# Optimization experiments

Measured on AMD Instinct MI355X. Metric: run time of the kernel, lower is better.

The kernel has to match this reference:

```python
import jax, jax.numpy as jnp
import numpy as np

B, T, H, I, O = 64, 1024, 512, 64, 8
NOISE_STD = 0.05
ALPHA = 0.2


def setup_inputs() -> dict:
    key = jax.random.key(0)
    ks = jax.random.split(key, 5)
    return {
        "input": jax.random.normal(ks[0], (B, T, I), dtype=jnp.float32),
        "noise": jax.random.normal(ks[1], (B, T, H), dtype=jnp.float32),
        "wi": jax.random.normal(ks[2], (I, H), dtype=jnp.float32) / np.float32(np.sqrt(H)),
        "si": jnp.ones((I,), jnp.float32),
        # scale so the all-positive effective recurrence |wrec| stays stable over T steps
        "wrec": jax.random.normal(ks[3], (H, H), dtype=jnp.float32) * np.float32(0.5 / H),
        "b": jnp.zeros((H,), jnp.float32),
        "wo": jax.random.normal(ks[4], (H, O), dtype=jnp.float32) / np.float32(H),
        "so": jnp.ones((O,), jnp.float32),
        "wi_mask": jnp.ones((I, H), jnp.float32),
        "wrec_mask": jnp.ones((H, H), jnp.float32),
        "wo_mask": jnp.ones((H, O), jnp.float32),
        "h0": jnp.zeros((H,), jnp.float32),
    }


def reference(input, noise, wi, si, wrec, b, wo, so, wi_mask, wrec_mask, wo_mask, h0):
    batch = input.shape[0]
    # effective weights (constant across timesteps; torch recomputes identical values each step)
    wrec_eff = jnp.abs(wrec) * wrec_mask            # [H, H]
    wi_eff = (wi * si[:, None]) * wi_mask           # [I, H]
    wo_eff = (wo * so[None, :]) * wo_mask           # [H, O]

    h_init = jnp.broadcast_to(h0, (batch, h0.shape[0]))  # [B, H]

    def step(h, xs):
        x_t, n_t = xs                                # [B, I], [B, H]
        r = jax.nn.relu(h)                           # rate from previous state
        h_new = h + NOISE_STD * n_t + ALPHA * (-h + r @ wrec_eff + b + x_t @ wi_eff)
        out_t = jax.nn.relu(h_new) @ wo_eff          # [B, O]
        return h_new, (out_t, h_new)

    xs = (jnp.swapaxes(input, 0, 1), jnp.swapaxes(noise, 0, 1))  # time-major
    _, (outs, hs) = jax.lax.scan(step, h_init, xs)
    output = jnp.swapaxes(outs, 0, 1)                            # [B, T, O]
    trajectories = jnp.concatenate(
        [h_init[:, None, :], jnp.swapaxes(hs, 0, 1)], axis=1     # [B, T+1, H]
    )
    return output, trajectories
```

## Files before the change

kernel.cpp:

```cpp
#include <hip/hip_runtime.h>
#include <hip/hip_bf16.h>
#include <cstddef>
#include <cstdint>

#define BB 64
#define TT 1024
#define HH 512
#define II 64
#define OO 8
#define NOISE_STD 0.05f
#define ALPHA 0.2f

#define G_SLICES 16
#define BT 4
#define NC (BB/BT)
#define K4EXT 160
#define R2STRIDE 328

typedef _Float16 half2_t __attribute__((ext_vector_type(2)));
typedef unsigned int uint32;
typedef uint32 uint4_t __attribute__((ext_vector_type(4)));

#if __has_builtin(__builtin_amdgcn_fdot2)
__device__ __forceinline__ float fdot2f(half2_t a, half2_t b, float c) {
    return __builtin_amdgcn_fdot2(a, b, c, false);
}
#else
__device__ __forceinline__ float fdot2f(half2_t a, half2_t b, float c) {
    return c + (float)a[0] * (float)b[0] + (float)a[1] * (float)b[1];
}
#endif

__device__ __forceinline__ half2_t pkrtz(float a, float b) {
    return __builtin_bit_cast(half2_t, __builtin_amdgcn_cvt_pkrtz(a, b));
}

__device__ __forceinline__ uint4_t load4_sc1(const uint32* p) {
    uint4_t v;
    asm volatile("global_load_dwordx4 %0, %1, off sc1\n\t"
                 "s_waitcnt vmcnt(0)"
                 : "=v"(v) : "v"(p) : "memory");
    return v;
}
__device__ __forceinline__ uint4_t load4_sc0(const uint32* p) {
    uint4_t v;
    asm volatile("global_load_dwordx4 %0, %1, off sc0\n\t"
                 "s_waitcnt vmcnt(0)"
                 : "=v"(v) : "v"(p) : "memory");
    return v;
}
__device__ __forceinline__ void store1_plain(uint32* p, uint32 v) {
    asm volatile("global_store_dword %0, %1, off" :: "v"(p), "v"(v) : "memory");
}

__global__ __launch_bounds__(512, 2)
void rnn_clique(const float* __restrict__ input, const float* __restrict__ noise,
                const float* __restrict__ wi, const float* __restrict__ si,
                const float* __restrict__ wrec, const float* __restrict__ bvec,
                const float* __restrict__ wo, const float* __restrict__ so,
                const float* __restrict__ wi_mask, const float* __restrict__ wrec_mask,
                const float* __restrict__ wo_mask, const float* __restrict__ h0,
                uint32* __restrict__ ex, float* __restrict__ out,
                float* __restrict__ traj)
{
    const int tid  = threadIdx.x;
    const int cq   = blockIdx.x & 15;
    const int sl   = blockIdx.x >> 4;
    const int wv   = tid >> 6;
    const int lane = tid & 63;

    __shared__ half2_t w2[K4EXT * 64];
    __shared__ half2_t r2[2][BT][R2STRIDE];
    __shared__ float   part[BT][8][32];
    __shared__ half2_t wo2[256];
    __shared__ int     mode_sh;

    uint32* aux = ex + (size_t)NC * 2 * BT * HH;

    if (tid == 0) {
        uint32 xcc;
        asm volatile("s_getreg_b32 %0, hwreg(HW_REG_XCC_ID)" : "=s"(xcc));
        xcc &= 0xFFu;
        __hip_atomic_store(aux + cq * 16 + sl, (1u << 16) | xcc,
                           __ATOMIC_RELAXED, __HIP_MEMORY_SCOPE_AGENT);
    }

    {
        const int c = tid & 31, kg = tid >> 5;
        const int gc = sl * 32 + c;
        for (int m = 0; m < 10; ++m) {
            int k4 = m * 16 + kg;
            float v[4];
            #pragma unroll
            for (int q = 0; q < 4; ++q) {
                int kap = k4 * 4 + q;
                float x;
                if (kap < HH) {
                    x = fabsf(wrec[(size_t)kap * HH + gc]) * wrec_mask[(size_t)kap * HH + gc];
                } else if (kap < HH + II) {
                    int i = kap - HH;
                    x = wi[(size_t)i * HH + gc] * si[i] * wi_mask[(size_t)i * HH + gc];
                } else if (kap == HH + II) {
                    x = bvec[gc];
                } else {
                    x = 0.f;
                }
                v[q] = x;
            }
            w2[k4 * 64 + c * 2]     = pkrtz(v[0], v[1]);
            w2[k4 * 64 + c * 2 + 1] = pkrtz(v[2], v[3]);
        }
    }
    if (sl < OO && tid < 256) {
        int k2 = tid, o = sl;
        float v0 = wo[(size_t)(2 * k2) * OO + o] * so[o] * wo_mask[(size_t)(2 * k2) * OO + o];
        float v1 = wo[(size_t)(2 * k2 + 1) * OO + o] * so[o] * wo_mask[(size_t)(2 * k2 + 1) * OO + o];
        wo2[k2] = pkrtz(v0, v1);
    }
    if (tid < 128) {
        int k4 = tid;
        float v0 = fmaxf(h0[4 * k4 + 0], 0.f), v1 = fmaxf(h0[4 * k4 + 1], 0.f);
        float v2 = fmaxf(h0[4 * k4 + 2], 0.f), v3 = fmaxf(h0[4 * k4 + 3], 0.f);
        half2_t p0 = pkrtz(v0, v1), p1 = pkrtz(v2, v3);
        for (int b = 0; b < BT; ++b) { r2[0][b][2 * k4] = p0; r2[0][b][2 * k4 + 1] = p1; }
    }
    if (tid < 8) {
        int par = tid & 1, b = tid >> 1;
        r2[par][b][288] = half2_t{(_Float16)1.f, (_Float16)0.f};
        for (int s = 289; s < R2STRIDE; ++s) r2[par][b][s] = half2_t{(_Float16)0.f, (_Float16)0.f};
    }
    if (wv >= 4 && lane < 32) {
        int b = wv - 4, i2 = lane;
        const float* xp = input + ((size_t)(cq * BT + b) * TT + 0) * II + 2 * i2;
        r2[0][b][256 + i2] = pkrtz(xp[0], xp[1]);
    }

    float h_st = 0.f, n_reg = 0.f, n_reg2 = 0.f;
    float* trajp = nullptr;
    const float* noisep = nullptr;
    uint32* exw = nullptr;
    if (wv < BT && lane < 32) {
        int b = wv, c = lane, gc = sl * 32 + c, bg = cq * BT + b;
        h_st   = h0[gc];
        noisep = noise + (size_t)bg * TT * HH;
        trajp  = traj + (size_t)bg * (TT + 1) * HH;
        n_reg  = noisep[gc];
        n_reg2 = noisep[(size_t)HH + gc];
        trajp[gc] = h_st;
        exw = ex + (size_t)(cq * 2 * BT + b) * HH + gc;
    }
    __syncthreads();

    const int c_    = lane & 31;
    const int shalf = lane >> 5;
    const int seg   = wv * 2 + shalf;

    half2_t wr[5][4];
    #pragma unroll
    for (int ch = 0; ch < 5; ++ch) {
        int k4b = seg * 10 + ch * 2;
        wr[ch][0] = w2[k4b * 64 + c_ * 2];
        wr[ch][1] = w2[k4b * 64 + c_ * 2 + 1];
        wr[ch][2] = w2[(k4b + 1) * 64 + c_ * 2];
        wr[ch][3] = w2[(k4b + 1) * 64 + c_ * 2 + 1];
    }

    if (wv == 0) {
        uint32 v = (1u << 16);
        for (;;) {
            if (lane < 16)
                v = __hip_atomic_load(aux + cq * 16 + lane,
                                      __ATOMIC_RELAXED, __HIP_MEMORY_SCOPE_AGENT);
            if (__ballot((v >> 16) == 1u) == ~0ull) break;
            __builtin_amdgcn_s_sleep(1);
        }
        uint32 myx = v & 0xFFFFu;
        uint32 x0  = __shfl(myx, 0);
        bool eq = (lane < 16) ? (myx == x0) : true;
        if (lane == 0) mode_sh = (__ballot(eq) == ~0ull) ? 1 : 0;
    }
    __syncthreads();
    const bool local_mode = (mode_sh != 0);

    const int gb  = tid >> 7;
    const int k4g = tid & 127;
    uint32* exg0 = ex + (size_t)(cq * 2 * BT + gb) * HH + (size_t)(4 * k4g);
    const size_t expar = (size_t)BT * HH;

    for (int t = 0; t < TT; ++t) {
        const int p = t & 1;

        float acc0 = 0.f, acc1 = 0.f, acc2 = 0.f, acc3 = 0.f;
        #pragma unroll
        for (int ch = 0; ch < 5; ++ch) {
            int k2b = seg * 20 + ch * 4;
            {
                half2_t ra = r2[p][0][k2b], rb = r2[p][0][k2b + 1], rc = r2[p][0][k2b + 2], rd = r2[p][0][k2b + 3];
                acc0 = fdot2f(ra, wr[ch][0], acc0); acc0 = fdot2f(rb, wr[ch][1], acc0);
                acc0 = fdot2f(rc, wr[ch][2], acc0); acc0 = fdot2f(rd, wr[ch][3], acc0);
            }
            {
                half2_t ra = r2[p][1][k2b], rb = r2[p][1][k2b + 1], rc = r2[p][1][k2b + 2], rd = r2[p][1][k2b + 3];
                acc1 = fdot2f(ra, wr[ch][0], acc1); acc1 = fdot2f(rb, wr[ch][1], acc1);
                acc1 = fdot2f(rc, wr[ch][2], acc1); acc1 = fdot2f(rd, wr[ch][3], acc1);
            }
            {
                half2_t ra = r2[p][2][k2b], rb = r2[p][2][k2b + 1], rc = r2[p][2][k2b + 2], rd = r2[p][2][k2b + 3];
                acc2 = fdot2f(ra, wr[ch][0], acc2); acc2 = fdot2f(rb, wr[ch][1], acc2);
                acc2 = fdot2f(rc, wr[ch][2], acc2); acc2 = fdot2f(rd, wr[ch][3], acc2);
            }
            {
                half2_t ra = r2[p][3][k2b], rb = r2[p][3][k2b + 1], rc = r2[p][3][k2b + 2], rd = r2[p][3][k2b + 3];
                acc3 = fdot2f(ra, wr[ch][0], acc3); acc3 = fdot2f(rb, wr[ch][1], acc3);
                acc3 = fdot2f(rc, wr[ch][2], acc3); acc3 = fdot2f(rd, wr[ch][3], acc3);
            }
        }
        acc0 += __shfl_xor(acc0, 32);
        acc1 += __shfl_xor(acc1, 32);
        acc2 += __shfl_xor(acc2, 32);
        acc3 += __shfl_xor(acc3, 32);
        if (shalf == 0) {
            part[0][wv][c_] = acc0;
            part[1][wv][c_] = acc1;
            part[2][wv][c_] = acc2;
            part[3][wv][c_] = acc3;
        }
        __syncthreads();

        const uint32 tag = (uint32)(t + 2);
        const size_t poff = (size_t)p * expar;

        if (wv < BT && lane < 32) {
            int b = wv, c = lane, gc = sl * 32 + c;
            float mv = 0.f;
            #pragma unroll
            for (int m = 0; m < 8; ++m) mv += part[b][m][c];
            float hn = (1.f - ALPHA) * h_st + ALPHA * mv + NOISE_STD * n_reg;
            h_st = hn;
            uint32 r16 = __builtin_bit_cast(uint32,
                           __builtin_amdgcn_cvt_pkrtz(fmaxf(hn, 0.f), 0.f)) & 0xFFFFu;
            uint32 word = (tag << 16) | r16;
            if (local_mode) {
                store1_plain(exw + poff, word);
            } else {
                __hip_atomic_store(exw + poff, word,
                                   __ATOMIC_RELAXED, __HIP_MEMORY_SCOPE_AGENT);
            }
            trajp[(size_t)(t + 1) * HH + gc] = hn;
            n_reg = n_reg2;
            int tn = (t + 2 < TT) ? (t + 2) : (TT - 1);
            n_reg2 = noisep[(size_t)tn * HH + gc];
        } else if (wv >= 4) {
            if (sl < OO && t > 0) {
                int b = wv - 4;
                int k2 = lane * 4;
                float q = 0.f;
                q = fdot2f(r2[p][b][k2],     wo2[k2],     q);
                q = fdot2f(r2[p][b][k2 + 1], wo2[k2 + 1], q);
                q = fdot2f(r2[p][b][k2 + 2], wo2[k2 + 2], q);
                q = fdot2f(r2[p][b][k2 + 3], wo2[k2 + 3], q);
                #pragma unroll
                for (int d = 32; d >= 1; d >>= 1) q += __shfl_xor(q, d);
                if (lane == 0) out[((size_t)(cq * BT + b) * TT + (t - 1)) * OO + sl] = q;
            }
            if (lane < 32) {
                int b = wv - 4, i2 = lane;
                int tn = (t + 1 < TT) ? (t + 1) : (TT - 1);
                const float* xp = input + ((size_t)(cq * BT + b) * TT + tn) * II + 2 * i2;
                r2[p ^ 1][b][256 + i2] = pkrtz(xp[0], xp[1]);
            }
        }

        {
            const uint32* g0 = exg0 + poff;
            uint4_t w;
            int spins = 0;
            if (local_mode) {
                for (;;) {
                    w = load4_sc0(g0);
                    if ((w[0] >> 16) == tag && (w[1] >> 16) == tag &&
                        (w[2] >> 16) == tag && (w[3] >> 16) == tag) break;
                    if (++spins > 8) __builtin_amdgcn_s_sleep(1);
                }
            } else {
                for (;;) {
                    w = load4_sc1(g0);
                    if ((w[0] >> 16) == tag && (w[1] >> 16) == tag &&
                        (w[2] >> 16) == tag && (w[3] >> 16) == tag) break;
                    __builtin_amdgcn_s_sleep(1);
                }
            }
            uint32 q0 = (w[0] & 0xFFFFu) | (w[1] << 16);
            uint32 q1 = (w[2] & 0xFFFFu) | (w[3] << 16);
            r2[p ^ 1][gb][2 * k4g]     = __builtin_bit_cast(half2_t, q0);
            r2[p ^ 1][gb][2 * k4g + 1] = __builtin_bit_cast(half2_t, q1);
        }
        __syncthreads();
    }

    if (wv >= 4 && sl < OO) {
        int b = wv - 4;
        int k2 = lane * 4;
        float q = 0.f;
        q = fdot2f(r2[0][b][k2],     wo2[k2],     q);
        q = fdot2f(r2[0][b][k2 + 1], wo2[k2 + 1], q);
        q = fdot2f(r2[0][b][k2 + 2], wo2[k2 + 2], q);
        q = fdot2f(r2[0][b][k2 + 3], wo2[k2 + 3], q);
        #pragma unroll
        for (int d = 32; d >= 1; d >>= 1) q += __shfl_xor(q, d);
        if (lane == 0) out[((size_t)(cq * BT + b) * TT + (TT - 1)) * OO + sl] = q;
    }
}

extern "C" void kernel_launch(void* const* d_in, const int* in_sizes, int n_in,
                              void* d_out, int out_size, void* d_ws, size_t ws_size,
                              hipStream_t stream) {
    const float* input     = (const float*)d_in[0];
    const float* noise     = (const float*)d_in[1];
    const float* wi        = (const float*)d_in[2];
    const float* si        = (const float*)d_in[3];
    const float* wrec      = (const float*)d_in[4];
    const float* bvec      = (const float*)d_in[5];
    const float* wo        = (const float*)d_in[6];
    const float* so        = (const float*)d_in[7];
    const float* wi_mask   = (const float*)d_in[8];
    const float* wrec_mask = (const float*)d_in[9];
    const float* wo_mask   = (const float*)d_in[10];
    const float* h0        = (const float*)d_in[11];

    float* out  = (float*)d_out;
    float* traj = out + (size_t)BB * TT * OO;
    uint32* ex  = (uint32*)d_ws;

    (void)hipMemsetAsync(d_ws, 0,
        (size_t)(NC * 2 * BT * HH + NC * G_SLICES) * sizeof(uint32), stream);

    rnn_clique<<<dim3(NC * G_SLICES), dim3(512), 0, stream>>>(
        input, noise, wi, si, wrec, bvec, wo, so,
        wi_mask, wrec_mask, wo_mask, h0, ex, out, traj);
}
```

Measured before the change: 1.602 ms.

## Offload noise, input and trajectory traffic to helper waves and use lighter barriers

```diff
diff --git a/kernel.cpp b/kernel.cpp
--- a/kernel.cpp
+++ b/kernel.cpp
@@ -33,6 +33,12 @@
 
 __device__ __forceinline__ half2_t pkrtz(float a, float b) {
     return __builtin_bit_cast(half2_t, __builtin_amdgcn_cvt_pkrtz(a, b));
+}
+
+__device__ __forceinline__ void barrier_lgkm() {
+    asm volatile("s_waitcnt lgkmcnt(0)" ::: "memory");
+    __builtin_amdgcn_s_barrier();
+    asm volatile("" ::: "memory");
 }
 
 __device__ __forceinline__ uint4_t load4_sc1(const uint32* p) {
@@ -73,6 +79,8 @@
     __shared__ half2_t r2[2][BT][R2STRIDE];
     __shared__ float   part[BT][8][32];
     __shared__ half2_t wo2[256];
+    __shared__ float   nbuf[3][BT][32];
+    __shared__ float   hbuf[2][BT][32];
     __shared__ int     mode_sh;
 
     uint32* aux = ex + (size_t)NC * 2 * BT * HH;
@@ -129,25 +137,30 @@
         r2[par][b][288] = half2_t{(_Float16)1.f, (_Float16)0.f};
         for (int s = 289; s < R2STRIDE; ++s) r2[par][b][s] = half2_t{(_Float16)0.f, (_Float16)0.f};
     }
-    if (wv >= 4 && lane < 32) {
-        int b = wv - 4, i2 = lane;
-        const float* xp = input + ((size_t)(cq * BT + b) * TT + 0) * II + 2 * i2;
-        r2[0][b][256 + i2] = pkrtz(xp[0], xp[1]);
-    }
-
-    float h_st = 0.f, n_reg = 0.f, n_reg2 = 0.f;
+
+    float h_st = 0.f;
     float* trajp = nullptr;
-    const float* noisep = nullptr;
     uint32* exw = nullptr;
     if (wv < BT && lane < 32) {
-        int b = wv, c = lane, gc = sl * 32 + c, bg = cq * BT + b;
-        h_st   = h0[gc];
-        noisep = noise + (size_t)bg * TT * HH;
-        trajp  = traj + (size_t)bg * (TT + 1) * HH;
-        n_reg  = noisep[gc];
-        n_reg2 = noisep[(size_t)HH + gc];
+        int b = wv, gc = sl * 32 + lane, bg = cq * BT + b;
+        h_st  = h0[gc];
+        trajp = traj + (size_t)bg * (TT + 1) * HH;
         trajp[gc] = h_st;
         exw = ex + (size_t)(cq * 2 * BT + b) * HH + gc;
+    }
+    const float* noisepb = nullptr;
+    const float* xbase = nullptr;
+    float* trajpb = nullptr;
+    int gcw = sl * 32 + (lane & 31);
+    if (wv >= 4 && lane < 32) {
+        int b = wv - 4, bg = cq * BT + b;
+        noisepb = noise + (size_t)bg * TT * HH;
+        xbase   = input + (size_t)bg * TT * II;
+        trajpb  = traj + (size_t)bg * (TT + 1) * HH;
+        nbuf[0][b][lane] = noisepb[gcw];
+        nbuf[1][b][lane] = noisepb[(size_t)HH + gcw];
+        const float* xp = xbase;
+        r2[0][b][256 + lane] = pkrtz(xp[2 * lane], xp[2 * lane + 1]);
     }
     __syncthreads();
 
@@ -189,6 +202,15 @@
 
     for (int t = 0; t < TT; ++t) {
         const int p = t & 1;
+
+        float nfly = 0.f, xa = 0.f, xb = 0.f;
+        if (wv >= 4 && lane < 32) {
+            int tn2 = (t + 2 < TT) ? (t + 2) : (TT - 1);
+            nfly = noisepb[(size_t)tn2 * HH + gcw];
+            int tn1 = (t + 1 < TT) ? (t + 1) : (TT - 1);
+            const float* xp = xbase + (size_t)tn1 * II;
+            xa = xp[2 * lane]; xb = xp[2 * lane + 1];
+        }
 
         float acc0 = 0.f, acc1 = 0.f, acc2 = 0.f, acc3 = 0.f;
         #pragma unroll
@@ -225,17 +247,17 @@
             part[2][wv][c_] = acc2;
             part[3][wv][c_] = acc3;
         }
-        __syncthreads();
+        barrier_lgkm();
 
         const uint32 tag = (uint32)(t + 2);
         const size_t poff = (size_t)p * expar;
 
         if (wv < BT && lane < 32) {
-            int b = wv, c = lane, gc = sl * 32 + c;
+            int b = wv;
             float mv = 0.f;
             #pragma unroll
-            for (int m = 0; m < 8; ++m) mv += part[b][m][c];
-            float hn = (1.f - ALPHA) * h_st + ALPHA * mv + NOISE_STD * n_reg;
+            for (int m = 0; m < 8; ++m) mv += part[b][m][c_];
+            float hn = (1.f - ALPHA) * h_st + ALPHA * mv + NOISE_STD * nbuf[t % 3][b][lane];
             h_st = hn;
             uint32 r16 = __builtin_bit_cast(uint32,
                            __builtin_amdgcn_cvt_pkrtz(fmaxf(hn, 0.f), 0.f)) & 0xFFFFu;
@@ -246,29 +268,7 @@
                 __hip_atomic_store(exw + poff, word,
                                    __ATOMIC_RELAXED, __HIP_MEMORY_SCOPE_AGENT);
             }
-            trajp[(size_t)(t + 1) * HH + gc] = hn;
-            n_reg = n_reg2;
-            int tn = (t + 2 < TT) ? (t + 2) : (TT - 1);
-            n_reg2 = noisep[(size_t)tn * HH + gc];
-        } else if (wv >= 4) {
-            if (sl < OO && t > 0) {
-                int b = wv - 4;
-                int k2 = lane * 4;
-                float q = 0.f;
-                q = fdot2f(r2[p][b][k2],     wo2[k2],     q);
-                q = fdot2f(r2[p][b][k2 + 1], wo2[k2 + 1], q);
-                q = fdot2f(r2[p][b][k2 + 2], wo2[k2 + 2], q);
-                q = fdot2f(r2[p][b][k2 + 3], wo2[k2 + 3], q);
-                #pragma unroll
-                for (int d = 32; d >= 1; d >>= 1) q += __shfl_xor(q, d);
-                if (lane == 0) out[((size_t)(cq * BT + b) * TT + (t - 1)) * OO + sl] = q;
-            }
-            if (lane < 32) {
-                int b = wv - 4, i2 = lane;
-                int tn = (t + 1 < TT) ? (t + 1) : (TT - 1);
-                const float* xp = input + ((size_t)(cq * BT + b) * TT + tn) * II + 2 * i2;
-                r2[p ^ 1][b][256 + i2] = pkrtz(xp[0], xp[1]);
-            }
+            hbuf[p ^ 1][b][lane] = hn;
         }
 
         {
@@ -295,9 +295,35 @@
             r2[p ^ 1][gb][2 * k4g]     = __builtin_bit_cast(half2_t, q0);
             r2[p ^ 1][gb][2 * k4g + 1] = __builtin_bit_cast(half2_t, q1);
         }
-        __syncthreads();
-    }
-
+
+        if (wv >= 4) {
+            if (sl < OO && t > 0) {
+                int b = wv - 4;
+                int k2 = lane * 4;
+                float q = 0.f;
+                q = fdot2f(r2[p][b][k2],     wo2[k2],     q);
+                q = fdot2f(r2[p][b][k2 + 1], wo2[k2 + 1], q);
+                q = fdot2f(r2[p][b][k2 + 2], wo2[k2 + 2], q);
+                q = fdot2f(r2[p][b][k2 + 3], wo2[k2 + 3], q);
+                #pragma unroll
+                for (int d = 32; d >= 1; d >>= 1) q += __shfl_xor(q, d);
+                if (lane == 0) out[((size_t)(cq * BT + (wv - 4)) * TT + (t - 1)) * OO + sl] = q;
+            }
+            if (lane < 32) {
+                int b = wv - 4;
+                r2[p ^ 1][b][256 + lane] = pkrtz(xa, xb);
+                nbuf[(t + 2) % 3][b][lane] = nfly;
+                if (t > 0)
+                    trajpb[(size_t)t * HH + gcw] = hbuf[p][b][lane];
+            }
+        }
+        barrier_lgkm();
+    }
+
+    if (wv >= 4 && lane < 32) {
+        int b = wv - 4;
+        trajpb[(size_t)TT * HH + gcw] = hbuf[0][b][lane];
+    }
     if (wv >= 4 && sl < OO) {
         int b = wv - 4;
         int k2 = lane * 4;
```

Measured after the change: 2.119 ms. +32.2%, slower.
